# Kernel tuning notes

Hardware: AMD Instinct MI355X
Metric: run time of the kernel (lower is better)

The kernel has to match this reference:

```python
import jax, jax.numpy as jnp
import numpy as np

BLOCK_M, BLOCK_K = 16, 64
THRES = 0.8


def setup_inputs() -> dict:
    key = jax.random.key(0)
    kx, kw = jax.random.split(key)
    bsz, seq, in_f, out_f = 128, 1, 4096, 11008
    x = jax.random.normal(kx, (bsz, seq, in_f), dtype=jnp.float16)
    # kaiming_uniform_(a=sqrt(5)) on a (in,out) weight -> bound = 1/sqrt(fan_in)
    bound = 1.0 / np.sqrt(in_f)
    weight = jax.random.uniform(kw, (in_f, out_f), dtype=jnp.float16,
                                minval=-bound, maxval=bound)
    bias = jnp.zeros((out_f,), dtype=jnp.float16)
    return {"x": x, "weight": weight, "bias": bias}


def reference(x, weight, bias):
    bsz, seq, hidden = x.shape
    x2 = x.reshape(bsz * seq, hidden)          # (M, K), seq == 1 decode path
    M, K = x2.shape
    # avg_magnitude_threshold: per (BLOCK_M, BLOCK_K) block mean |x| vs thres
    blocks = x2.reshape(M // BLOCK_M, BLOCK_M, K // BLOCK_K, BLOCK_K)
    avg = jnp.mean(jnp.abs(blocks).astype(jnp.float32), axis=(1, 3))  # (M/bm, K/bk)
    mask = avg > THRES                           # block active if avg magnitude above thres
    # blocksparse_masked_gemm: skipped blocks contribute nothing -> zero them out
    xm = jnp.where(mask[:, None, :, None], blocks, jnp.float16(0)).reshape(M, K)
    y = xm @ weight                              # (M, out_features)
    return y.reshape(bsz, seq, -1) + bias
```

## Files before the change

### kernel.cpp

```cpp
#include <hip/hip_runtime.h>
#include <stdint.h>

using f32x4   = __attribute__((ext_vector_type(4))) float;
using short8  = __attribute__((ext_vector_type(8))) short;
using float4v = __attribute__((ext_vector_type(4))) float;
using float2v = __attribute__((ext_vector_type(2))) float;
using uint2v  = __attribute__((ext_vector_type(2))) unsigned int;
using uint4v  = __attribute__((ext_vector_type(4))) unsigned int;

#define NCOL 11008
#define KDIM 4096
#define BSTRIDE 72

__device__ __forceinline__ unsigned pk_bf16(float a, float b) {
  unsigned ua = __float_as_uint(a); ua += 0x7fffu + ((ua >> 16) & 1u);
  unsigned ub = __float_as_uint(b); ub += 0x7fffu + ((ub >> 16) & 1u);
  return (ua >> 16) | (ub & 0xffff0000u);
}

__global__ __launch_bounds__(256) void mask_convert_kernel(
    const float* __restrict__ x, unsigned* __restrict__ xbf) {
  const int rb = blockIdx.x;
  const int g  = blockIdx.y;
  const int t  = threadIdx.x;
  __shared__ double part[256];
  __shared__ unsigned sh_bits;

  const float* base = x + (size_t)rb * 16 * KDIM + g * 512 + t * 2;
  double s = 0.0;
#pragma unroll
  for (int r = 0; r < 16; ++r) {
    float2v a = *(const float2v*)(base + (size_t)r * KDIM);
    s += (double)fabsf(a[0]) + (double)fabsf(a[1]);
  }
  part[t] = s;
  __syncthreads();
  if (t < 8) {
    double acc = 0.0;
#pragma unroll
    for (int u = 0; u < 32; ++u) acc += part[t * 32 + u];
    bool on = (acc * (1.0 / 1024.0)) > (double)0.8f;
    unsigned long long bal = __ballot(on);
    if (t == 0) sh_bits = (unsigned)(bal & 0xffu);
  }
  __syncthreads();
  const unsigned keep = (sh_bits >> (t >> 5)) & 1u;

  unsigned* dst = xbf + (size_t)rb * 16 * (KDIM / 2) + g * 256 + t;
#pragma unroll
  for (int r = 0; r < 16; ++r) {
    float2v a = *(const float2v*)(base + (size_t)r * KDIM);
    dst[(size_t)r * (KDIM / 2)] = keep ? pk_bf16(a[0], a[1]) : 0u;
  }
}

__global__ __launch_bounds__(256) void gemm_kernel(
    const unsigned* __restrict__ xbf, const float* __restrict__ w,
    const float* __restrict__ bias, float* __restrict__ out) {

  __shared__ __align__(16) uint8_t lds[2 * 64 * BSTRIDE];

  const int tid  = threadIdx.x;
  const int lane = tid & 63;
  const int wv   = tid >> 6;
  const int c    = lane & 15;
  const int q    = lane >> 4;
  const int n0   = blockIdx.x * 32;

  f32x4 acc[2][2] = {};

  const int sk = tid >> 3;
  const int sn = (tid & 7) * 4;
  const size_t wOff = (size_t)sk * NCOL + n0 + sn;

  auto issueW = [&](int kbi, float4v& r0, float4v& r1) {
    const float* wp = w + (size_t)kbi * 64 * NCOL + wOff;
    r0 = *(const float4v*)(wp);
    r1 = *(const float4v*)(wp + (size_t)32 * NCOL);
  };
  auto storeW = [&](uint8_t* buf, const float4v& r0, const float4v& r1) {
    uint2v v;
    v[0] = pk_bf16(r0[0], r0[1]);
    v[1] = pk_bf16(r0[2], r0[3]);
    *(uint2v*)(buf + (size_t)sk * BSTRIDE + sn * 2) = v;
    uint2v u;
    u[0] = pk_bf16(r1[0], r1[1]);
    u[1] = pk_bf16(r1[2], r1[3]);
    *(uint2v*)(buf + (size_t)(sk + 32) * BSTRIDE + sn * 2) = u;
  };

  const uint4v* aB0 = (const uint4v*)xbf + (size_t)((wv * 2 + 0) * 16 + c) * (KDIM / 8) + q;
  const uint4v* aB1 = (const uint4v*)xbf + (size_t)((wv * 2 + 1) * 16 + c) * (KDIM / 8) + q;

  auto loadA = [&](int kbi, uint4v* AR) {
    AR[0] = aB0[kbi * 8 + 0];
    AR[1] = aB0[kbi * 8 + 4];
    AR[2] = aB1[kbi * 8 + 0];
    AR[3] = aB1[kbi * 8 + 4];
  };

  auto compute = [&](const uint8_t* buf, const uint4v* AR) {
#pragma unroll
    for (int ks = 0; ks < 2; ++ks) {
      union { uint4v u; short8 v; } a0, a1;
      a0.u = AR[ks];
      a1.u = AR[2 + ks];

      const uint8_t* wb = buf + (size_t)(ks * 32 + q * 8) * BSTRIDE + c * 4;
      unsigned wj[8];
#pragma unroll
      for (int j = 0; j < 8; ++j)
        wj[j] = *(const unsigned*)(wb + (size_t)j * BSTRIDE);
      union { short8 v; unsigned u[4]; } be, bo;
#pragma unroll
      for (int pp = 0; pp < 4; ++pp) {
        be.u[pp] = (wj[2 * pp] & 0x0000ffffu) | (wj[2 * pp + 1] << 16);
        bo.u[pp] = (wj[2 * pp] >> 16) | (wj[2 * pp + 1] & 0xffff0000u);
      }
      acc[0][0] = __builtin_amdgcn_mfma_f32_16x16x32_bf16(a0.v, be.v, acc[0][0], 0, 0, 0);
      acc[0][1] = __builtin_amdgcn_mfma_f32_16x16x32_bf16(a0.v, bo.v, acc[0][1], 0, 0, 0);
      acc[1][0] = __builtin_amdgcn_mfma_f32_16x16x32_bf16(a1.v, be.v, acc[1][0], 0, 0, 0);
      acc[1][1] = __builtin_amdgcn_mfma_f32_16x16x32_bf16(a1.v, bo.v, acc[1][1], 0, 0, 0);
    }
  };

#define BAR()                                             \
  {                                                       \
    asm volatile("s_waitcnt lgkmcnt(0)" ::: "memory");    \
    __builtin_amdgcn_s_barrier();                         \
  }

  uint4v aC[4], aN[4];
  float4v wa0, wa1, wb0, wb1;
  issueW(0, wa0, wa1);
  loadA(0, aC);
  issueW(1, wb0, wb1);
  loadA(1, aN);

  uint8_t* const bufE = lds;
  uint8_t* const bufO = lds + 64 * BSTRIDE;

  for (int kb = 0; kb < 62; kb += 2) {
    storeW(bufE, wa0, wa1);
    issueW(kb + 2, wa0, wa1);
    BAR();
    compute(bufE, aC);
    loadA(kb + 2, aC);
    storeW(bufO, wb0, wb1);
    issueW(kb + 3, wb0, wb1);
    BAR();
    compute(bufO, aN);
    loadA(kb + 3, aN);
  }
  storeW(bufE, wa0, wa1);
  BAR();
  compute(bufE, aC);
  storeW(bufO, wb0, wb1);
  BAR();
  compute(bufO, aN);
#undef BAR

  const int colE = n0 + 2 * c;
  const float bE = bias[colE];
  const float bO = bias[colE + 1];
#pragma unroll
  for (int b = 0; b < 2; ++b) {
#pragma unroll
    for (int pp = 0; pp < 4; ++pp) {
      const int row = (wv * 2 + b) * 16 + q * 4 + pp;
      float2v st;
      st[0] = acc[b][0][pp] + bE;
      st[1] = acc[b][1][pp] + bO;
      *(float2v*)(out + (size_t)row * NCOL + colE) = st;
    }
  }
}

extern "C" void kernel_launch(void* const* d_in, const int* in_sizes, int n_in,
                              void* d_out, int out_size, void* d_ws, size_t ws_size,
                              hipStream_t stream) {
  const float* x    = (const float*)d_in[0];
  const float* w    = (const float*)d_in[1];
  const float* bias = (const float*)d_in[2];
  float* out        = (float*)d_out;
  unsigned* xbf     = (unsigned*)d_ws;

  hipLaunchKernelGGL(mask_convert_kernel, dim3(8, 8), dim3(256), 0, stream, x, xbf);
  hipLaunchKernelGGL(gemm_kernel, dim3(344), dim3(256), 0, stream,
                     xbf, w, bias, out);
}
```

Measured before the change: 294.3 us.

## Split GEMM along K into four segments with atomic accumulation

Adds a second grid dimension so each block handles a quarter of the K range, raising the block count to better fill the GPU while streaming the weight matrix. Partial sums are combined with relaxed fp32 atomic adds into the output, which a new kernel pre-initializes with the bias. This trades extra output traffic, atomics and a launch for more parallelism, and makes the summation order nondeterministic.

Result: no change. 289.9 us (-1.5%).

```diff
diff --git a/kernel.cpp b/kernel.cpp
--- a/kernel.cpp
+++ b/kernel.cpp
@@ -11,6 +11,8 @@
 #define NCOL 11008
 #define KDIM 4096
 #define BSTRIDE 72
+#define KSEG 4
+#define KB_PER_SEG 16
 
 __device__ __forceinline__ unsigned pk_bf16(float a, float b) {
   unsigned ua = __float_as_uint(a); ua += 0x7fffu + ((ua >> 16) & 1u);
@@ -54,9 +56,15 @@
   }
 }
 
+__global__ __launch_bounds__(256) void bias_init_kernel(
+    const float* __restrict__ bias, float* __restrict__ out) {
+  const int n = blockIdx.x * 256 + threadIdx.x;
+  out[(size_t)blockIdx.y * NCOL + n] = bias[n];
+}
+
 __global__ __launch_bounds__(256) void gemm_kernel(
     const unsigned* __restrict__ xbf, const float* __restrict__ w,
-    const float* __restrict__ bias, float* __restrict__ out) {
+    float* __restrict__ out) {
 
   __shared__ __align__(16) uint8_t lds[2 * 64 * BSTRIDE];
 
@@ -66,6 +74,7 @@
   const int c    = lane & 15;
   const int q    = lane >> 4;
   const int n0   = blockIdx.x * 32;
+  const int kb0  = blockIdx.y * KB_PER_SEG;
 
   f32x4 acc[2][2] = {};
 
@@ -132,15 +141,15 @@
 
   uint4v aC[4], aN[4];
   float4v wa0, wa1, wb0, wb1;
-  issueW(0, wa0, wa1);
-  loadA(0, aC);
-  issueW(1, wb0, wb1);
-  loadA(1, aN);
+  issueW(kb0 + 0, wa0, wa1);
+  loadA(kb0 + 0, aC);
+  issueW(kb0 + 1, wb0, wb1);
+  loadA(kb0 + 1, aN);
 
   uint8_t* const bufE = lds;
   uint8_t* const bufO = lds + 64 * BSTRIDE;
 
-  for (int kb = 0; kb < 62; kb += 2) {
+  for (int kb = kb0; kb < kb0 + KB_PER_SEG - 2; kb += 2) {
     storeW(bufE, wa0, wa1);
     issueW(kb + 2, wa0, wa1);
     BAR();
@@ -161,17 +170,16 @@
 #undef BAR
 
   const int colE = n0 + 2 * c;
-  const float bE = bias[colE];
-  const float bO = bias[colE + 1];
 #pragma unroll
   for (int b = 0; b < 2; ++b) {
 #pragma unroll
     for (int pp = 0; pp < 4; ++pp) {
       const int row = (wv * 2 + b) * 16 + q * 4 + pp;
-      float2v st;
-      st[0] = acc[b][0][pp] + bE;
-      st[1] = acc[b][1][pp] + bO;
-      *(float2v*)(out + (size_t)row * NCOL + colE) = st;
+      float* p = out + (size_t)row * NCOL + colE;
+      __hip_atomic_fetch_add(p,     acc[b][0][pp], __ATOMIC_RELAXED,
+                             __HIP_MEMORY_SCOPE_AGENT);
+      __hip_atomic_fetch_add(p + 1, acc[b][1][pp], __ATOMIC_RELAXED,
+                             __HIP_MEMORY_SCOPE_AGENT);
     }
   }
 }
@@ -186,6 +194,7 @@
   unsigned* xbf     = (unsigned*)d_ws;
 
   hipLaunchKernelGGL(mask_convert_kernel, dim3(8, 8), dim3(256), 0, stream, x, xbf);
-  hipLaunchKernelGGL(gemm_kernel, dim3(344), dim3(256), 0, stream,
-                     xbf, w, bias, out);
-}
+  hipLaunchKernelGGL(bias_init_kernel, dim3(43, 128), dim3(256), 0, stream, bias, out);
+  hipLaunchKernelGGL(gemm_kernel, dim3(344, KSEG), dim3(256), 0, stream,
+                     xbf, w, out);
+}
```
